# Performance work log

Measured on AMD Instinct MI355X. Metric: run time of the kernel, lower is better.

## Reference

```python
import jax, jax.numpy as jnp
import numpy as np

N_NODES = 200000
N_EDGES = 6400000
N_GRAPHS = 1000


def setup_inputs() -> dict:
    key = jax.random.key(0)
    ks = jax.random.split(key, 8)
    x = jax.random.normal(ks[0], (N_NODES, 2), dtype=jnp.float32)
    edge_index = jax.random.randint(ks[1], (2, N_EDGES), 0, N_NODES, dtype=jnp.int32)
    batch = jnp.sort(jax.random.randint(ks[2], (N_NODES,), 0, N_GRAPHS, dtype=jnp.int32))
    W1 = jax.random.normal(ks[3], (2, 16), dtype=jnp.float32) * (1.0 / np.sqrt(2))
    b1 = jnp.zeros((16,), jnp.float32)
    W2 = jax.random.normal(ks[4], (16, 32), dtype=jnp.float32) * (1.0 / np.sqrt(16))
    b2 = jnp.zeros((32,), jnp.float32)
    Wfc1 = jax.random.normal(ks[5], (32, 16), dtype=jnp.float32) * (1.0 / np.sqrt(32))
    bfc1 = jnp.zeros((16,), jnp.float32)
    Wfc2 = jax.random.normal(ks[6], (16, 1), dtype=jnp.float32) * (1.0 / np.sqrt(16))
    bfc2 = jnp.zeros((1,), jnp.float32)
    return {"x": x, "edge_index": edge_index, "batch": batch,
            "W1": W1, "b1": b1, "W2": W2, "b2": b2,
            "Wfc1": Wfc1, "bfc1": bfc1, "Wfc2": Wfc2, "bfc2": bfc2}


def _gcn_norm(edge_index, n_nodes):
    # PyG GCNConv default: add self loops, symmetric normalization.
    loops = jnp.arange(n_nodes, dtype=edge_index.dtype)
    src = jnp.concatenate([edge_index[0], loops])  # message source (row)
    dst = jnp.concatenate([edge_index[1], loops])  # aggregation target (col)
    deg = jax.ops.segment_sum(jnp.ones_like(dst, jnp.float32), dst, num_segments=n_nodes)
    dinv = jnp.where(deg > 0, jax.lax.rsqrt(jnp.maximum(deg, 1.0)), 0.0)
    norm = dinv[src] * dinv[dst]  # [E + N]
    return src, dst, norm


def _gcn_conv(h, W, b, src, dst, norm, n_nodes):
    h = h @ W                                      # transform first (small width)
    msg = h[src] * norm[:, None]                   # gather + scale: [E+N, F]
    out = jax.ops.segment_sum(msg, dst, num_segments=n_nodes)
    return out + b


def reference(x, edge_index, batch, W1, b1, W2, b2, Wfc1, bfc1, Wfc2, bfc2):
    n = x.shape[0]
    src, dst, norm = _gcn_norm(edge_index, n)
    h = jax.nn.relu(_gcn_conv(x, W1, b1, src, dst, norm, n))
    h = jax.nn.relu(_gcn_conv(h, W2, b2, src, dst, norm, n))
    # global_mean_pool over graph ids
    sums = jax.ops.segment_sum(h, batch, num_segments=N_GRAPHS)
    cnts = jax.ops.segment_sum(jnp.ones((n,), h.dtype), batch, num_segments=N_GRAPHS)
    pooled = sums / jnp.maximum(cnts, 1.0)[:, None]  # [G, 32]
    out = jax.nn.relu(pooled @ Wfc1 + bfc1)
    out = out @ Wfc2 + bfc2                          # [G, 1]
    return out.squeeze(-1)
```

## Files before the change

kernel.cpp:

```cpp
#include <hip/hip_runtime.h>
#include <hip/hip_fp16.h>

static inline size_t align256(size_t x) { return (x + 255) & ~size_t(255); }

#define CAP 36864

__global__ __launch_bounds__(512) void k_scatter(const int* __restrict__ ei,
                                                 int* __restrict__ bcursor,
                                                 unsigned* __restrict__ bdata, int E) {
    __shared__ int lcount[256];
    __shared__ int gbase[256];
    int t = threadIdx.x;
    if (t < 256) lcount[t] = 0;
    __syncthreads();
    int chunk = blockIdx.x * 8192;
    int srcv[16], bkt[16], rank[16], dl[16];
#pragma unroll
    for (int k = 0; k < 16; ++k) {
        int e = chunk + k * 512 + t;
        bkt[k] = -1;
        if (e < E) {
            int sv = ei[e], d = ei[E + e];
            int b = d >> 10;
            srcv[k] = sv; bkt[k] = b; dl[k] = d & 1023;
            rank[k] = atomicAdd(&lcount[b], 1);
        }
    }
    __syncthreads();
    if (t < 256) {
        int c = lcount[t];
        gbase[t] = t * CAP + (c ? atomicAdd(&bcursor[t], c) : 0);
    }
    __syncthreads();
#pragma unroll
    for (int k = 0; k < 16; ++k) {
        if (bkt[k] >= 0)
            bdata[gbase[bkt[k]] + rank[k]] = ((unsigned)dl[k] << 18) | (unsigned)srcv[k];
    }
}

__global__ void k_bscan2(const int* __restrict__ bcursor, int* __restrict__ bbase,
                         int NBv, int E) {
    __shared__ int lds[256];
    int t = threadIdx.x;
    int v = (t < NBv) ? bcursor[t] : 0;
    lds[t] = v;
    __syncthreads();
    for (int off = 1; off < 256; off <<= 1) {
        int x = (t >= off) ? lds[t - off] : 0;
        __syncthreads();
        lds[t] += x;
        __syncthreads();
    }
    if (t < NBv) bbase[t] = lds[t] - v;
    if (t == 0) bbase[NBv] = E;
}

__global__ __launch_bounds__(1024) void k_build(const unsigned* __restrict__ bdata,
                                                const int* __restrict__ bbase,
                                                int* __restrict__ row_ptr,
                                                float* __restrict__ dinv,
                                                int* __restrict__ col,
                                                const float* __restrict__ x,
                                                float2* __restrict__ xt,
                                                int N, int E, int NBv) {
    __shared__ int curs[1024];
    __shared__ int sums[256];
    __shared__ int stage[CAP];
    int* hist = stage;
    int bkt = blockIdx.x;
    int t = threadIdx.x;
    int tb = bbase[bkt];
    int count = bbase[bkt + 1] - tb;
    int fs = bkt * CAP;
    int node0 = bkt << 10;
    int nn = N - node0; if (nn > 1024) nn = 1024;
    hist[t] = 0;
    __syncthreads();
    for (int e = t; e < count; e += 1024)
        atomicAdd(&hist[bdata[fs + e] >> 18], 1);
    __syncthreads();
    int v0 = 0, v1 = 0, v2 = 0, v3 = 0, s = 0;
    if (t < 256) {
        int b4 = t * 4;
        v0 = hist[b4]; v1 = hist[b4 + 1]; v2 = hist[b4 + 2]; v3 = hist[b4 + 3];
        s = v0 + v1 + v2 + v3;
        sums[t] = s;
    }
    __syncthreads();
    for (int off = 1; off < 256; off <<= 1) {
        int xv = 0;
        if (t < 256 && t >= off) xv = sums[t - off];
        __syncthreads();
        if (t < 256) sums[t] += xv;
        __syncthreads();
    }
    if (t < 256) {
        int b4 = t * 4;
        int e0 = sums[t] - s;
        int e1 = e0 + v0, e2 = e1 + v1, e3 = e2 + v2;
        curs[b4] = e0; curs[b4 + 1] = e1; curs[b4 + 2] = e2; curs[b4 + 3] = e3;
        if (b4 < nn)     { row_ptr[node0 + b4]     = tb + e0; dinv[node0 + b4]     = rsqrtf((float)v0 + 1.f); }
        if (b4 + 1 < nn) { row_ptr[node0 + b4 + 1] = tb + e1; dinv[node0 + b4 + 1] = rsqrtf((float)v1 + 1.f); }
        if (b4 + 2 < nn) { row_ptr[node0 + b4 + 2] = tb + e2; dinv[node0 + b4 + 2] = rsqrtf((float)v2 + 1.f); }
        if (b4 + 3 < nn) { row_ptr[node0 + b4 + 3] = tb + e3; dinv[node0 + b4 + 3] = rsqrtf((float)v3 + 1.f); }
    }
    if (bkt == NBv - 1 && t == 0) row_ptr[N] = E;
    __syncthreads();
    for (int e = t; e < count; e += 1024) {
        unsigned p = bdata[fs + e];
        int dl = p >> 18;
        int pos = atomicAdd(&curs[dl], 1);
        stage[pos] = (int)(p & 0x3FFFFu);
    }
    __syncthreads();
    for (int i = t; i < count; i += 1024)
        col[tb + i] = stage[i];
    for (int i = t; i < nn; i += 1024) {
        int node = node0 + i;
        float d2 = dinv[node];
        xt[node] = make_float2(x[node * 2] * d2, x[node * 2 + 1] * d2);
    }
}

__global__ __launch_bounds__(256) void k_conv1_fused(const int* __restrict__ rp,
                                                     const int* __restrict__ col,
                                                     const float2* __restrict__ xt,
                                                     const float* __restrict__ dinv,
                                                     const float* __restrict__ W1,
                                                     const float* __restrict__ b1,
                                                     uint2* __restrict__ ht, int n) {
    int gt = blockIdx.x * 256 + threadIdx.x;
    int node = gt >> 2;
    int q = gt & 3;
    if (node >= n) return;
    int rs = rp[node], re = rp[node + 1];
    float a0 = 0.f, a1 = 0.f;
    int e = rs + q;
    for (; e + 12 < re; e += 16) {
        int c0 = __builtin_nontemporal_load(col + e);
        int c1 = __builtin_nontemporal_load(col + e + 4);
        int c2 = __builtin_nontemporal_load(col + e + 8);
        int c3 = __builtin_nontemporal_load(col + e + 12);
        float2 v0 = xt[c0];
        float2 v1 = xt[c1];
        float2 v2 = xt[c2];
        float2 v3 = xt[c3];
        a0 += (v0.x + v1.x) + (v2.x + v3.x);
        a1 += (v0.y + v1.y) + (v2.y + v3.y);
    }
    for (; e < re; e += 4) {
        float2 v = xt[__builtin_nontemporal_load(col + e)];
        a0 += v.x; a1 += v.y;
    }
    if (q == 0) { float2 sf = xt[node]; a0 += sf.x; a1 += sf.y; }
    a0 += __shfl_xor(a0, 1); a0 += __shfl_xor(a0, 2);
    a1 += __shfl_xor(a1, 1); a1 += __shfl_xor(a1, 2);
    float dv = dinv[node];
    a0 *= dv; a1 *= dv;
    int f0 = q * 4;
    float v0 = fmaxf(a0 * W1[f0]     + a1 * W1[16 + f0]     + b1[f0],     0.f) * dv;
    float v1 = fmaxf(a0 * W1[f0 + 1] + a1 * W1[16 + f0 + 1] + b1[f0 + 1], 0.f) * dv;
    float v2 = fmaxf(a0 * W1[f0 + 2] + a1 * W1[16 + f0 + 2] + b1[f0 + 2], 0.f) * dv;
    float v3 = fmaxf(a0 * W1[f0 + 3] + a1 * W1[16 + f0 + 3] + b1[f0 + 3], 0.f) * dv;
    __half2 h0 = __floats2half2_rn(v0, v1);
    __half2 h1 = __floats2half2_rn(v2, v3);
    uint2 w;
    w.x = *reinterpret_cast<unsigned*>(&h0);
    w.y = *reinterpret_cast<unsigned*>(&h1);
    ht[(size_t)node * 4 + q] = w;
}

__global__ __launch_bounds__(256) void k_gather2(const int* __restrict__ rp,
                                                 const int* __restrict__ col,
                                                 const __half2* __restrict__ ht,
                                                 const float* __restrict__ dinv,
                                                 float* __restrict__ agg, int N) {
    int gt = blockIdx.x * 256 + threadIdx.x;
    int node = gt >> 3;
    int fq = gt & 7;
    if (node >= N) return;
    int rs = rp[node], re = rp[node + 1];
    const __half2* __restrict__ base = ht + fq;
    float ax = 0.f, ay = 0.f;
    int e = rs;
    for (; e + 16 <= re; e += 16) {
        int c[16];
#pragma unroll
        for (int k = 0; k < 16; ++k) c[k] = __builtin_nontemporal_load(col + e + k);
        float2 v[16];
#pragma unroll
        for (int k = 0; k < 16; ++k) v[k] = __half22float2(base[(size_t)c[k] * 8]);
#pragma unroll
        for (int k = 0; k < 16; ++k) { ax += v[k].x; ay += v[k].y; }
    }
    for (; e + 8 <= re; e += 8) {
        int c[8];
#pragma unroll
        for (int k = 0; k < 8; ++k) c[k] = __builtin_nontemporal_load(col + e + k);
        float2 v[8];
#pragma unroll
        for (int k = 0; k < 8; ++k) v[k] = __half22float2(base[(size_t)c[k] * 8]);
#pragma unroll
        for (int k = 0; k < 8; ++k) { ax += v[k].x; ay += v[k].y; }
    }
    for (; e < re; ++e) {
        float2 v = __half22float2(base[(size_t)col[e] * 8]);
        ax += v.x; ay += v.y;
    }
    {
        float2 v = __half22float2(base[(size_t)node * 8]);
        ax += v.x; ay += v.y;
    }
    float dv = dinv[node];
    __builtin_nontemporal_store(ax * dv, agg + (size_t)node * 16 + 2 * fq);
    __builtin_nontemporal_store(ay * dv, agg + (size_t)node * 16 + 2 * fq + 1);
}

__global__ __launch_bounds__(256) void k_trans_pool(const float* __restrict__ agg,
                                                    const float* __restrict__ W2,
                                                    const float* __restrict__ b2,
                                                    const int* __restrict__ batch,
                                                    float* __restrict__ gsum, int N) {
    __shared__ float aggs[64][17];
    __shared__ float h2s[64][33];
    __shared__ float w2s[512];
    __shared__ float b2s[32];
    __shared__ int   bids[64];
    int t = threadIdx.x;
    if (t < 128) ((float4*)w2s)[t] = ((const float4*)W2)[t];
    if (t < 32)  b2s[t] = b2[t];
    int node0 = blockIdx.x * 64;
    if (t < 64)  bids[t] = (node0 + t < N) ? batch[node0 + t] : -1;
    {
        int nl = t >> 2, q = t & 3;
        int node = node0 + nl;
        float4 v = make_float4(0.f, 0.f, 0.f, 0.f);
        if (node < N) v = *(const float4*)(agg + (size_t)node * 16 + (size_t)q * 4);
        int c0 = q * 4;
        aggs[nl][c0] = v.x; aggs[nl][c0 + 1] = v.y;
        aggs[nl][c0 + 2] = v.z; aggs[nl][c0 + 3] = v.w;
    }
    __syncthreads();
    {
        int nl = t >> 2;
        int jq = (t & 3) * 8;
        float o[8];
#pragma unroll
        for (int j = 0; j < 8; ++j) o[j] = b2s[jq + j];
#pragma unroll
        for (int k = 0; k < 16; ++k) {
            float a = aggs[nl][k];
#pragma unroll
            for (int j = 0; j < 8; ++j) o[j] += a * w2s[k * 32 + jq + j];
        }
#pragma unroll
        for (int j = 0; j < 8; ++j) h2s[nl][jq + j] = fmaxf(o[j], 0.f);
    }
    __syncthreads();
    if (t < 128) {
        int j = t & 31, seg = t >> 5;
        int nbeg = seg * 16, nend = nbeg + 16;
        float acc = 0.f;
        int cur = bids[nbeg];
        for (int n2 = nbeg; n2 < nend; ++n2) {
            int b = bids[n2];
            if (b != cur) {
                if (cur >= 0) atomicAdd(&gsum[(size_t)cur * 32 + j], acc);
                acc = 0.f; cur = b;
            }
            if (b >= 0) acc += h2s[n2][j];
        }
        if (cur >= 0) atomicAdd(&gsum[(size_t)cur * 32 + j], acc);
    }
}

__global__ void k_starts(const int* __restrict__ batch, int* __restrict__ start,
                         int n, int G) {
    int i = blockIdx.x * blockDim.x + threadIdx.x;
    if (i >= n) return;
    int b = batch[i];
    int bp = (i == 0) ? -1 : batch[i - 1];
    for (int k = bp + 1; k <= b; ++k) start[k] = i;
    if (i == n - 1) {
        for (int k = b + 1; k <= G; ++k) start[k] = n;
    }
}

__global__ void k_final(const float* __restrict__ gsum, const int* __restrict__ start,
                        const float* __restrict__ Wfc1, const float* __restrict__ bfc1,
                        const float* __restrict__ Wfc2, const float* __restrict__ bfc2,
                        float* __restrict__ out, int G) {
    int g = blockIdx.x * blockDim.x + threadIdx.x;
    if (g >= G) return;
    float cnt = (float)(start[g + 1] - start[g]);
    float inv = 1.f / fmaxf(cnt, 1.f);
    float p[32];
#pragma unroll
    for (int i = 0; i < 32; ++i) p[i] = gsum[(size_t)g * 32 + i] * inv;
    float o = bfc2[0];
#pragma unroll
    for (int j = 0; j < 16; ++j) {
        float a = bfc1[j];
#pragma unroll
        for (int i = 0; i < 32; ++i) a += p[i] * Wfc1[i * 16 + j];
        o += fmaxf(a, 0.f) * Wfc2[j];
    }
    out[g] = o;
}

extern "C" void kernel_launch(void* const* d_in, const int* in_sizes, int n_in,
                              void* d_out, int out_size, void* d_ws, size_t ws_size,
                              hipStream_t stream) {
    const float* x     = (const float*)d_in[0];
    const int*   ei    = (const int*)d_in[1];
    const int*   batch = (const int*)d_in[2];
    const float* W1    = (const float*)d_in[3];
    const float* b1    = (const float*)d_in[4];
    const float* W2    = (const float*)d_in[5];
    const float* b2    = (const float*)d_in[6];
    const float* Wfc1  = (const float*)d_in[7];
    const float* bfc1  = (const float*)d_in[8];
    const float* Wfc2  = (const float*)d_in[9];
    const float* bfc2  = (const float*)d_in[10];
    float* out = (float*)d_out;

    const int N = in_sizes[0] / 2;
    const int E = in_sizes[1] / 2;
    const int G = out_size;
    const int NBv = (N + 1023) >> 10;

    char* ws = (char*)d_ws;
    size_t off = 0;
    float* dinv    = (float*)(ws + off); off += align256((size_t)N * 4);
    int*   row_ptr = (int*)(ws + off);   off += align256((size_t)(N + 1) * 4);
    int*   bcursor = (int*)(ws + off);   off += align256(256 * 4);
    int*   bbase   = (int*)(ws + off);   off += align256(257 * 4);
    int*   start   = (int*)(ws + off);   off += align256((size_t)(G + 1) * 4);
    float* gsum    = (float*)(ws + off); off += align256((size_t)G * 32 * 4);
    float2* xt     = (float2*)(ws + off); off += align256((size_t)N * 8);
    __half2* ht    = (__half2*)(ws + off); off += align256((size_t)N * 32);
    float* agg     = (float*)(ws + off); off += align256((size_t)N * 16 * 4);
    int*   col     = (int*)(ws + off);   off += align256((size_t)E * 4);
    unsigned* bdata = (unsigned*)(ws + off); off += align256((size_t)NBv * CAP * 4);

    const int BS = 256;

    hipMemsetAsync(bcursor, 0, 256 * 4, stream);
    hipMemsetAsync(gsum, 0, (size_t)G * 32 * 4, stream);

    k_scatter<<<(E + 8191) / 8192, 512, 0, stream>>>(ei, bcursor, bdata, E);
    k_bscan2<<<1, 256, 0, stream>>>(bcursor, bbase, NBv, E);
    k_build<<<NBv, 1024, 0, stream>>>(bdata, bbase, row_ptr, dinv, col, x, xt, N, E, NBv);

    k_conv1_fused<<<((size_t)N * 4 + 255) / 256, 256, 0, stream>>>(row_ptr, col, xt, dinv,
                                                                   W1, b1, (uint2*)ht, N);
    k_gather2<<<((size_t)N * 8 + 255) / 256, 256, 0, stream>>>(row_ptr, col, ht, dinv, agg, N);
    k_trans_pool<<<(N + 63) / 64, 256, 0, stream>>>(agg, W2, b2, batch, gsum, N);

    k_starts<<<(N + BS - 1) / BS, BS, 0, stream>>>(batch, start, N, G);
    k_final<<<(G + BS - 1) / BS, BS, 0, stream>>>(gsum, start, Wfc1, bfc1, Wfc2, bfc2, out, G);
}
```

Before: 254.9 us.

## Widen layer-2 gather to 16-byte loads and fold graph-start computation into final kernel

The second-layer gather now gives each node two threads instead of eight, and each thread loads a full 16-byte uint4 (eight half features) per neighbor rather than one half2. This cuts the number of gather instructions and the redundant col index loads per edge, which should ease the latency-bound random gathers, at the cost of fewer threads in flight and more registers per thread. Separately, the k_starts kernel is removed and k_final finds each graph's node count by binary searching the sorted batch array. That saves one kernel launch.

```diff
diff --git a/kernel.cpp b/kernel.cpp
--- a/kernel.cpp
+++ b/kernel.cpp
@@ -173,48 +173,62 @@
 
 __global__ __launch_bounds__(256) void k_gather2(const int* __restrict__ rp,
                                                  const int* __restrict__ col,
-                                                 const __half2* __restrict__ ht,
+                                                 const uint4* __restrict__ ht,
                                                  const float* __restrict__ dinv,
                                                  float* __restrict__ agg, int N) {
     int gt = blockIdx.x * 256 + threadIdx.x;
-    int node = gt >> 3;
-    int fq = gt & 7;
+    int node = gt >> 1;
+    int hf = gt & 1;
     if (node >= N) return;
     int rs = rp[node], re = rp[node + 1];
-    const __half2* __restrict__ base = ht + fq;
-    float ax = 0.f, ay = 0.f;
+    const uint4* __restrict__ base = ht + hf;
+    float s0 = 0.f, s1 = 0.f, s2 = 0.f, s3 = 0.f, s4 = 0.f, s5 = 0.f, s6 = 0.f, s7 = 0.f;
     int e = rs;
-    for (; e + 16 <= re; e += 16) {
-        int c[16];
-#pragma unroll
-        for (int k = 0; k < 16; ++k) c[k] = __builtin_nontemporal_load(col + e + k);
-        float2 v[16];
-#pragma unroll
-        for (int k = 0; k < 16; ++k) v[k] = __half22float2(base[(size_t)c[k] * 8]);
-#pragma unroll
-        for (int k = 0; k < 16; ++k) { ax += v[k].x; ay += v[k].y; }
-    }
     for (; e + 8 <= re; e += 8) {
         int c[8];
 #pragma unroll
         for (int k = 0; k < 8; ++k) c[k] = __builtin_nontemporal_load(col + e + k);
-        float2 v[8];
-#pragma unroll
-        for (int k = 0; k < 8; ++k) v[k] = __half22float2(base[(size_t)c[k] * 8]);
-#pragma unroll
-        for (int k = 0; k < 8; ++k) { ax += v[k].x; ay += v[k].y; }
+        uint4 u[8];
+#pragma unroll
+        for (int k = 0; k < 8; ++k) u[k] = base[(size_t)c[k] * 2];
+#pragma unroll
+        for (int k = 0; k < 8; ++k) {
+            float2 f0 = __half22float2(*reinterpret_cast<__half2*>(&u[k].x));
+            float2 f1 = __half22float2(*reinterpret_cast<__half2*>(&u[k].y));
+            float2 f2 = __half22float2(*reinterpret_cast<__half2*>(&u[k].z));
+            float2 f3 = __half22float2(*reinterpret_cast<__half2*>(&u[k].w));
+            s0 += f0.x; s1 += f0.y; s2 += f1.x; s3 += f1.y;
+            s4 += f2.x; s5 += f2.y; s6 += f3.x; s7 += f3.y;
+        }
     }
     for (; e < re; ++e) {
-        float2 v = __half22float2(base[(size_t)col[e] * 8]);
-        ax += v.x; ay += v.y;
+        uint4 u = base[(size_t)__builtin_nontemporal_load(col + e) * 2];
+        float2 f0 = __half22float2(*reinterpret_cast<__half2*>(&u.x));
+        float2 f1 = __half22float2(*reinterpret_cast<__half2*>(&u.y));
+        float2 f2 = __half22float2(*reinterpret_cast<__half2*>(&u.z));
+        float2 f3 = __half22float2(*reinterpret_cast<__half2*>(&u.w));
+        s0 += f0.x; s1 += f0.y; s2 += f1.x; s3 += f1.y;
+        s4 += f2.x; s5 += f2.y; s6 += f3.x; s7 += f3.y;
     }
     {
-        float2 v = __half22float2(base[(size_t)node * 8]);
-        ax += v.x; ay += v.y;
+        uint4 u = base[(size_t)node * 2];
+        float2 f0 = __half22float2(*reinterpret_cast<__half2*>(&u.x));
+        float2 f1 = __half22float2(*reinterpret_cast<__half2*>(&u.y));
+        float2 f2 = __half22float2(*reinterpret_cast<__half2*>(&u.z));
+        float2 f3 = __half22float2(*reinterpret_cast<__half2*>(&u.w));
+        s0 += f0.x; s1 += f0.y; s2 += f1.x; s3 += f1.y;
+        s4 += f2.x; s5 += f2.y; s6 += f3.x; s7 += f3.y;
     }
     float dv = dinv[node];
-    __builtin_nontemporal_store(ax * dv, agg + (size_t)node * 16 + 2 * fq);
-    __builtin_nontemporal_store(ay * dv, agg + (size_t)node * 16 + 2 * fq + 1);
+    float* dst = agg + (size_t)node * 16 + hf * 8;
+    __builtin_nontemporal_store(s0 * dv, dst);
+    __builtin_nontemporal_store(s1 * dv, dst + 1);
+    __builtin_nontemporal_store(s2 * dv, dst + 2);
+    __builtin_nontemporal_store(s3 * dv, dst + 3);
+    __builtin_nontemporal_store(s4 * dv, dst + 4);
+    __builtin_nontemporal_store(s5 * dv, dst + 5);
+    __builtin_nontemporal_store(s6 * dv, dst + 6);
+    __builtin_nontemporal_store(s7 * dv, dst + 7);
 }
 
 __global__ __launch_bounds__(256) void k_trans_pool(const float* __restrict__ agg,
@@ -275,25 +289,18 @@
     }
 }
 
-__global__ void k_starts(const int* __restrict__ batch, int* __restrict__ start,
-                         int n, int G) {
-    int i = blockIdx.x * blockDim.x + threadIdx.x;
-    if (i >= n) return;
-    int b = batch[i];
-    int bp = (i == 0) ? -1 : batch[i - 1];
-    for (int k = bp + 1; k <= b; ++k) start[k] = i;
-    if (i == n - 1) {
-        for (int k = b + 1; k <= G; ++k) start[k] = n;
-    }
-}
-
-__global__ void k_final(const float* __restrict__ gsum, const int* __restrict__ start,
+__global__ void k_final(const float* __restrict__ gsum, const int* __restrict__ batch,
                         const float* __restrict__ Wfc1, const float* __restrict__ bfc1,
                         const float* __restrict__ Wfc2, const float* __restrict__ bfc2,
-                        float* __restrict__ out, int G) {
+                        float* __restrict__ out, int G, int N) {
     int g = blockIdx.x * blockDim.x + threadIdx.x;
     if (g >= G) return;
-    float cnt = (float)(start[g + 1] - start[g]);
+    int lo = 0, hi = N;
+    while (lo < hi) { int m = (lo + hi) >> 1; if (batch[m] < g) lo = m + 1; else hi = m; }
+    int s = lo;
+    lo = s; hi = N;
+    while (lo < hi) { int m = (lo + hi) >> 1; if (batch[m] < g + 1) lo = m + 1; else hi = m; }
+    float cnt = (float)(lo - s);
     float inv = 1.f / fmaxf(cnt, 1.f);
     float p[32];
 #pragma unroll
@@ -336,7 +343,6 @@
     int*   row_ptr = (int*)(ws + off);   off += align256((size_t)(N + 1) * 4);
     int*   bcursor = (int*)(ws + off);   off += align256(256 * 4);
     int*   bbase   = (int*)(ws + off);   off += align256(257 * 4);
-    int*   start   = (int*)(ws + off);   off += align256((size_t)(G + 1) * 4);
     float* gsum    = (float*)(ws + off); off += align256((size_t)G * 32 * 4);
     float2* xt     = (float2*)(ws + off); off += align256((size_t)N * 8);
     __half2* ht    = (__half2*)(ws + off); off += align256((size_t)N * 32);
@@ -355,9 +361,10 @@
 
     k_conv1_fused<<<((size_t)N * 4 + 255) / 256, 256, 0, stream>>>(row_ptr, col, xt, dinv,
                                                                    W1, b1, (uint2*)ht, N);
-    k_gather2<<<((size_t)N * 8 + 255) / 256, 256, 0, stream>>>(row_ptr, col, ht, dinv, agg, N);
+    k_gather2<<<((size_t)N * 2 + 255) / 256, 256, 0, stream>>>(row_ptr, col, (const uint4*)ht,
+                                                               dinv, agg, N);
     k_trans_pool<<<(N + 63) / 64, 256, 0, stream>>>(agg, W2, b2, batch, gsum, N);
 
-    k_starts<<<(N + BS - 1) / BS, BS, 0, stream>>>(batch, start, N, G);
-    k_final<<<(G + BS - 1) / BS, BS, 0, stream>>>(gsum, start, Wfc1, bfc1, Wfc2, bfc2, out, G);
-}
+    k_final<<<(G + BS - 1) / BS, BS, 0, stream>>>(gsum, batch, Wfc1, bfc1, Wfc2, bfc2,
+                                                  out, G, N);
+}
```

Result: slower. 271.7 us (+6.6%).

## Fold bucket scan into build, binary-search graph counts, merge memsets, widen scatter

Applied to the files above, without the earlier changes.

Removes the separate bucket-scan kernel and recomputes the 256-entry prefix scan redundantly inside each k_build block. Drops the k_starts kernel and has k_final binary-search the sorted batch array for per-graph counts. Merges the two memsets into one contiguous zeroing. k_scatter now runs 1024 threads per block with int2 vector loads over 16K-edge chunks. The aim is fewer launches and less launch and serialization overhead, in exchange for some redundant scan work per block and higher register/LDS pressure in the scatter kernel.

```diff
diff --git a/kernel.cpp b/kernel.cpp
--- a/kernel.cpp
+++ b/kernel.cpp
@@ -5,25 +5,28 @@
 
 #define CAP 36864
 
-__global__ __launch_bounds__(512) void k_scatter(const int* __restrict__ ei,
-                                                 int* __restrict__ bcursor,
-                                                 unsigned* __restrict__ bdata, int E) {
+__global__ __launch_bounds__(1024) void k_scatter(const int* __restrict__ ei,
+                                                  int* __restrict__ bcursor,
+                                                  unsigned* __restrict__ bdata, int E) {
     __shared__ int lcount[256];
     __shared__ int gbase[256];
     int t = threadIdx.x;
     if (t < 256) lcount[t] = 0;
     __syncthreads();
-    int chunk = blockIdx.x * 8192;
+    int chunk = blockIdx.x * 16384;
     int srcv[16], bkt[16], rank[16], dl[16];
 #pragma unroll
-    for (int k = 0; k < 16; ++k) {
-        int e = chunk + k * 512 + t;
-        bkt[k] = -1;
+    for (int k = 0; k < 8; ++k) {
+        int e = chunk + k * 2048 + 2 * t;
+        int k2 = 2 * k;
+        bkt[k2] = -1; bkt[k2 + 1] = -1;
         if (e < E) {
-            int sv = ei[e], d = ei[E + e];
-            int b = d >> 10;
-            srcv[k] = sv; bkt[k] = b; dl[k] = d & 1023;
-            rank[k] = atomicAdd(&lcount[b], 1);
+            int2 sp = *(const int2*)(ei + e);
+            int2 dp = *(const int2*)(ei + E + e);
+            srcv[k2] = sp.x; bkt[k2] = dp.x >> 10; dl[k2] = dp.x & 1023;
+            rank[k2] = atomicAdd(&lcount[bkt[k2]], 1);
+            srcv[k2 + 1] = sp.y; bkt[k2 + 1] = dp.y >> 10; dl[k2 + 1] = dp.y & 1023;
+            rank[k2 + 1] = atomicAdd(&lcount[bkt[k2 + 1]], 1);
         }
     }
     __syncthreads();
@@ -39,25 +42,8 @@
     }
 }
 
-__global__ void k_bscan2(const int* __restrict__ bcursor, int* __restrict__ bbase,
-                         int NBv, int E) {
-    __shared__ int lds[256];
-    int t = threadIdx.x;
-    int v = (t < NBv) ? bcursor[t] : 0;
-    lds[t] = v;
-    __syncthreads();
-    for (int off = 1; off < 256; off <<= 1) {
-        int x = (t >= off) ? lds[t - off] : 0;
-        __syncthreads();
-        lds[t] += x;
-        __syncthreads();
-    }
-    if (t < NBv) bbase[t] = lds[t] - v;
-    if (t == 0) bbase[NBv] = E;
-}
-
 __global__ __launch_bounds__(1024) void k_build(const unsigned* __restrict__ bdata,
-                                                const int* __restrict__ bbase,
+                                                const int* __restrict__ bcursor,
                                                 int* __restrict__ row_ptr,
                                                 float* __restrict__ dinv,
                                                 int* __restrict__ col,
@@ -66,12 +52,22 @@
                                                 int N, int E, int NBv) {
     __shared__ int curs[1024];
     __shared__ int sums[256];
+    __shared__ int bsc[256];
     __shared__ int stage[CAP];
     int* hist = stage;
     int bkt = blockIdx.x;
     int t = threadIdx.x;
-    int tb = bbase[bkt];
-    int count = bbase[bkt + 1] - tb;
+    if (t < 256) bsc[t] = (t < NBv) ? bcursor[t] : 0;
+    __syncthreads();
+    for (int off = 1; off < 256; off <<= 1) {
+        int xv = 0;
+        if (t < 256 && t >= off) xv = bsc[t - off];
+        __syncthreads();
+        if (t < 256) bsc[t] += xv;
+        __syncthreads();
+    }
+    int count = bcursor[bkt];
+    int tb = bsc[bkt] - count;
     int fs = bkt * CAP;
     int node0 = bkt << 10;
     int nn = N - node0; if (nn > 1024) nn = 1024;
@@ -275,25 +271,18 @@
     }
 }
 
-__global__ void k_starts(const int* __restrict__ batch, int* __restrict__ start,
-                         int n, int G) {
-    int i = blockIdx.x * blockDim.x + threadIdx.x;
-    if (i >= n) return;
-    int b = batch[i];
-    int bp = (i == 0) ? -1 : batch[i - 1];
-    for (int k = bp + 1; k <= b; ++k) start[k] = i;
-    if (i == n - 1) {
-        for (int k = b + 1; k <= G; ++k) start[k] = n;
-    }
-}
-
-__global__ void k_final(const float* __restrict__ gsum, const int* __restrict__ start,
+__global__ void k_final(const float* __restrict__ gsum, const int* __restrict__ batch,
                         const float* __restrict__ Wfc1, const float* __restrict__ bfc1,
                         const float* __restrict__ Wfc2, const float* __restrict__ bfc2,
-                        float* __restrict__ out, int G) {
+                        float* __restrict__ out, int G, int N) {
     int g = blockIdx.x * blockDim.x + threadIdx.x;
     if (g >= G) return;
-    float cnt = (float)(start[g + 1] - start[g]);
+    int lo = 0, hi = N;
+    while (lo < hi) { int m = (lo + hi) >> 1; if (batch[m] < g) lo = m + 1; else hi = m; }
+    int s = lo;
+    lo = s; hi = N;
+    while (lo < hi) { int m = (lo + hi) >> 1; if (batch[m] < g + 1) lo = m + 1; else hi = m; }
+    float cnt = (float)(lo - s);
     float inv = 1.f / fmaxf(cnt, 1.f);
     float p[32];
 #pragma unroll
@@ -334,10 +323,9 @@
     size_t off = 0;
     float* dinv    = (float*)(ws + off); off += align256((size_t)N * 4);
     int*   row_ptr = (int*)(ws + off);   off += align256((size_t)(N + 1) * 4);
-    int*   bcursor = (int*)(ws + off);   off += align256(256 * 4);
-    int*   bbase   = (int*)(ws + off);   off += align256(257 * 4);
-    int*   start   = (int*)(ws + off);   off += align256((size_t)(G + 1) * 4);
+    int*   bcursor = (int*)(ws + off);   size_t z0 = off; off += align256(256 * 4);
     float* gsum    = (float*)(ws + off); off += align256((size_t)G * 32 * 4);
+    size_t zlen = off - z0;
     float2* xt     = (float2*)(ws + off); off += align256((size_t)N * 8);
     __half2* ht    = (__half2*)(ws + off); off += align256((size_t)N * 32);
     float* agg     = (float*)(ws + off); off += align256((size_t)N * 16 * 4);
@@ -346,18 +334,16 @@
 
     const int BS = 256;
 
-    hipMemsetAsync(bcursor, 0, 256 * 4, stream);
-    hipMemsetAsync(gsum, 0, (size_t)G * 32 * 4, stream);
-
-    k_scatter<<<(E + 8191) / 8192, 512, 0, stream>>>(ei, bcursor, bdata, E);
-    k_bscan2<<<1, 256, 0, stream>>>(bcursor, bbase, NBv, E);
-    k_build<<<NBv, 1024, 0, stream>>>(bdata, bbase, row_ptr, dinv, col, x, xt, N, E, NBv);
+    hipMemsetAsync(bcursor, 0, zlen, stream);
+
+    k_scatter<<<(E + 16383) / 16384, 1024, 0, stream>>>(ei, bcursor, bdata, E);
+    k_build<<<NBv, 1024, 0, stream>>>(bdata, bcursor, row_ptr, dinv, col, x, xt, N, E, NBv);
 
     k_conv1_fused<<<((size_t)N * 4 + 255) / 256, 256, 0, stream>>>(row_ptr, col, xt, dinv,
                                                                    W1, b1, (uint2*)ht, N);
     k_gather2<<<((size_t)N * 8 + 255) / 256, 256, 0, stream>>>(row_ptr, col, ht, dinv, agg, N);
     k_trans_pool<<<(N + 63) / 64, 256, 0, stream>>>(agg, W2, b2, batch, gsum, N);
 
-    k_starts<<<(N + BS - 1) / BS, BS, 0, stream>>>(batch, start, N, G);
-    k_final<<<(G + BS - 1) / BS, BS, 0, stream>>>(gsum, start, Wfc1, bfc1, Wfc2, bfc2, out, G);
-}
+    k_final<<<(G + BS - 1) / BS, BS, 0, stream>>>(gsum, batch, Wfc1, bfc1, Wfc2, bfc2,
+                                                  out, G, N);
+}
```

Result: faster. 244.4 us (-4.1%).
